# Kernel optimization log

Hardware: AMD Instinct MI355X
Metric: run time of the kernel (lower is better)

## Reference

```python
import jax, jax.numpy as jnp
import numpy as np

B, T, D, H = 2, 2048, 1024, 16
HS = D // H  # head_size = 64
DFF = 4 * D


def setup_inputs() -> dict:
    key = jax.random.key(0)
    ks = jax.random.split(key, 12)
    s = 0.02
    return {
        "x": jax.random.normal(ks[0], (B, T, D), dtype=jnp.float32),
        "Wq": jax.random.normal(ks[1], (D, D), dtype=jnp.float32) * s,
        "Wk": jax.random.normal(ks[2], (D, D), dtype=jnp.float32) * s,
        "Wv": jax.random.normal(ks[3], (D, D), dtype=jnp.float32) * s,
        "Wo": jax.random.normal(ks[4], (D, D), dtype=jnp.float32) * s,
        "bo": jnp.zeros((D,), dtype=jnp.float32),
        "W1": jax.random.normal(ks[5], (D, DFF), dtype=jnp.float32) * s,
        "b1": jnp.zeros((DFF,), dtype=jnp.float32),
        "W2": jax.random.normal(ks[6], (DFF, D), dtype=jnp.float32) * s,
        "b2": jnp.zeros((D,), dtype=jnp.float32),
        "g1": jnp.ones((D,), dtype=jnp.float32),
        "be1": jnp.zeros((D,), dtype=jnp.float32),
        "g2": jnp.ones((D,), dtype=jnp.float32),
        "be2": jnp.zeros((D,), dtype=jnp.float32),
    }


def layer_norm(x, g, b, eps=1e-5):
    mu = jnp.mean(x, axis=-1, keepdims=True)
    var = jnp.var(x, axis=-1, keepdims=True)
    return (x - mu) * jax.lax.rsqrt(var + eps) * g + b


def attention(x, Wq, Wk, Wv, Wo, bo):
    # x: [B,T,D] -> q,k,v: [B,H,T,HS]
    def split_heads(y):
        return y.reshape(B, T, H, HS).transpose(0, 2, 1, 3)
    q = split_heads(x @ Wq)
    k = split_heads(x @ Wk)
    v = split_heads(x @ Wv)
    scores = jnp.einsum("bhqd,bhkd->bhqk", q, k) / jnp.sqrt(jnp.float32(HS))
    causal = jnp.tril(jnp.ones((T, T), dtype=bool))
    scores = jnp.where(causal, scores, -jnp.inf)
    probs = jax.nn.softmax(scores, axis=-1)
    out = jnp.einsum("bhqk,bhkd->bhqd", probs, v)
    out = out.transpose(0, 2, 1, 3).reshape(B, T, D)
    return out @ Wo + bo


def reference(x, Wq, Wk, Wv, Wo, bo, W1, b1, W2, b2, g1, be1, g2, be2):
    x = x + attention(layer_norm(x, g1, be1), Wq, Wk, Wv, Wo, bo)
    h = layer_norm(x, g2, be2)
    x = x + (jax.nn.relu(h @ W1 + b1) @ W2 + b2)
    return x
```

## Files before the change

kernel.cpp:

```cpp
#include <hip/hip_runtime.h>
#include <stdint.h>

#define Bc   2
#define Tc   2048
#define Dc   1024
#define Hc   16
#define HSc  64
#define DFFc 4096
#define Mc   (Bc * Tc)

using f32x4 = __attribute__((ext_vector_type(4))) float;
using s16x8 = __attribute__((ext_vector_type(8))) short;

__device__ __forceinline__ ushort f2bf(float f) {
  union { float f; uint32_t u; } v; v.f = f;
  uint32_t r = (v.u + 0x7FFFu + ((v.u >> 16) & 1u)) >> 16;
  return (ushort)r;
}
__device__ __forceinline__ float bf2f(ushort u) {
  union { uint32_t u; float f; } v; v.u = ((uint32_t)u) << 16;
  return v.f;
}
__device__ __forceinline__ uint32_t cvtpk(float a, float b) {
  uint32_t r;
  asm volatile("v_cvt_pk_bf16_f32 %0, %1, %2" : "=v"(r) : "v"(a), "v"(b));
  return r;
}
__device__ __forceinline__ float wredsum(float v) {
#pragma unroll
  for (int o = 32; o > 0; o >>= 1) v += __shfl_down(v, o);
  return v;
}

__device__ __forceinline__ void gload16(const ushort* g, ushort* l) {
  __builtin_amdgcn_global_load_lds(
      (const __attribute__((address_space(1))) void*)g,
      (__attribute__((address_space(3))) void*)l, 16, 0, 0);
}

template <int N> __device__ __forceinline__ void vwait() {
  if constexpr (N == 0) asm volatile("s_waitcnt vmcnt(0)" ::: "memory");
  else if constexpr (N == 3) asm volatile("s_waitcnt vmcnt(3)" ::: "memory");
  else if constexpr (N == 4) asm volatile("s_waitcnt vmcnt(4)" ::: "memory");
  else if constexpr (N == 6) asm volatile("s_waitcnt vmcnt(6)" ::: "memory");
  else if constexpr (N == 8) asm volatile("s_waitcnt vmcnt(8)" ::: "memory");
}

__global__ __launch_bounds__(256) void tcast_all_kernel(
    const float* __restrict__ Wq, const float* __restrict__ Wk,
    const float* __restrict__ Wv, const float* __restrict__ Wo,
    const float* __restrict__ W1, const float* __restrict__ W2,
    ushort* __restrict__ wqkvt, ushort* __restrict__ wot,
    ushort* __restrict__ w1t, ushort* __restrict__ w2t) {
  __shared__ float t[32][33];
  const int id = blockIdx.x;
  const float* src; ushort* dst; int K, N, bx, by;
  if (id < 4096) {
    const int which = id >> 10, local = id & 1023;
    src = (which == 0) ? Wq : (which == 1) ? Wk : (which == 2) ? Wv : Wo;
    dst = (which == 3) ? wot : wqkvt + (size_t)which * 1024 * 1024;
    K = 1024; N = 1024; bx = local & 31; by = local >> 5;
  } else if (id < 8192) {
    const int local = id - 4096;
    src = W1; dst = w1t; K = 1024; N = 4096;
    bx = local & 127; by = local >> 7;
  } else {
    const int local = id - 8192;
    src = W2; dst = w2t; K = 4096; N = 1024;
    bx = local & 31; by = local >> 5;
  }
  const int tid = threadIdx.x;
  const int n0 = bx * 32, k0 = by * 32;
  const int r = tid >> 3, c4 = (tid & 7) * 4;
  const float4 v = *(const float4*)&src[(size_t)(k0 + r) * N + n0 + c4];
  t[r][c4] = v.x; t[r][c4 + 1] = v.y; t[r][c4 + 2] = v.z; t[r][c4 + 3] = v.w;
  __syncthreads();
  ushort4 o;
  o.x = f2bf(t[c4 + 0][r]); o.y = f2bf(t[c4 + 1][r]);
  o.z = f2bf(t[c4 + 2][r]); o.w = f2bf(t[c4 + 3][r]);
  *(ushort4*)&dst[(size_t)(n0 + r) * K + k0 + c4] = o;
}

__global__ __launch_bounds__(256) void ln_kernel(const float* __restrict__ x,
                                                 const float* __restrict__ g,
                                                 const float* __restrict__ b,
                                                 ushort* __restrict__ out) {
  const int row = blockIdx.x;
  const int tid = threadIdx.x;
  const int lane = tid & 63, wave = tid >> 6;
  const float4 v = ((const float4*)(x + (size_t)row * Dc))[tid];
  float s  = v.x + v.y + v.z + v.w;
  float s2 = v.x * v.x + v.y * v.y + v.z * v.z + v.w * v.w;
  __shared__ float rs[4], rs2[4];
  s = wredsum(s); s2 = wredsum(s2);
  if (lane == 0) { rs[wave] = s; rs2[wave] = s2; }
  __syncthreads();
  const float S  = rs[0] + rs[1] + rs[2] + rs[3];
  const float S2 = rs2[0] + rs2[1] + rs2[2] + rs2[3];
  const float mu = S * (1.f / (float)Dc);
  const float rstd = rsqrtf(S2 * (1.f / (float)Dc) - mu * mu + 1e-5f);
  const float4 gv = ((const float4*)g)[tid];
  const float4 bv = ((const float4*)b)[tid];
  ushort4 o;
  o.x = f2bf((v.x - mu) * rstd * gv.x + bv.x);
  o.y = f2bf((v.y - mu) * rstd * gv.y + bv.y);
  o.z = f2bf((v.z - mu) * rstd * gv.z + bv.z);
  o.w = f2bf((v.w - mu) * rstd * gv.w + bv.w);
  ((ushort4*)(out + (size_t)row * Dc))[tid] = o;
}

template <int BM, int NSPLIT, int OUT_BF16, int RELU, int BIAS, int RES, int QKVSPLIT>
__global__ __launch_bounds__(256) void gemm3_kernel(
    const ushort* __restrict__ A, const ushort* __restrict__ Bt,
    const float* __restrict__ bias, const float* __restrict__ res,
    void* __restrict__ C0, void* __restrict__ C1, void* __restrict__ C2,
    int M, int N, int K) {
  constexpr int MF = BM / 32;
  __shared__ __align__(16) ushort As[BM * 64];
  __shared__ __align__(16) ushort Bs[128 * 64];
  const int tid = threadIdx.x;
  const int lane = tid & 63, w = tid >> 6;
  const int wm = w >> 1, wn = w & 1;
  const int row0 = blockIdx.x * BM, col0 = blockIdx.y * 128;
  const int fr = lane & 15, fg = lane >> 4;
  const int kbeg = (NSPLIT > 1) ? blockIdx.z * (K / NSPLIT) : 0;
  const int kend = (NSPLIT > 1) ? kbeg + K / NSPLIT : K;

  f32x4 acc[MF][4] = {};

  for (int k0 = kbeg; k0 < kend; k0 += 64) {
#pragma unroll
    for (int i = 0; i < BM * 8 / 256; i++) {
      const int c = i * 256 + tid;
      const int r = c >> 3, j = c & 7;
      gload16(A + (size_t)(row0 + r) * K + k0 + ((j ^ (r & 7)) << 3),
              As + (i * 256 + w * 64) * 8);
    }
#pragma unroll
    for (int i = 0; i < 4; i++) {
      const int c = i * 256 + tid;
      const int r = c >> 3, j = c & 7;
      gload16(Bt + (size_t)(col0 + r) * K + k0 + ((j ^ (r & 7)) << 3),
              Bs + (i * 256 + w * 64) * 8);
    }
    __syncthreads();

#pragma unroll
    for (int kk = 0; kk < 2; kk++) {
      const int js = ((kk * 4 + fg) ^ (fr & 7)) << 3;
      s16x8 af[MF], bfr[4];
#pragma unroll
      for (int m = 0; m < MF; m++)
        af[m] = *(const s16x8*)&As[(wm * (BM / 2) + m * 16 + fr) * 64 + js];
#pragma unroll
      for (int n = 0; n < 4; n++)
        bfr[n] = *(const s16x8*)&Bs[(wn * 64 + n * 16 + fr) * 64 + js];
#pragma unroll
      for (int m = 0; m < MF; m++)
#pragma unroll
        for (int n = 0; n < 4; n++)
          acc[m][n] = __builtin_amdgcn_mfma_f32_16x16x32_bf16(af[m], bfr[n], acc[m][n], 0, 0, 0);
    }
    __syncthreads();
  }

  if (NSPLIT > 1) {
    float* P = (float*)C0 + (size_t)blockIdx.z * M * N;
#pragma unroll
    for (int m = 0; m < MF; m++)
#pragma unroll
      for (int n = 0; n < 4; n++)
#pragma unroll
        for (int i = 0; i < 4; i++) {
          const int r = row0 + wm * (BM / 2) + m * 16 + fg * 4 + i;
          const int c = col0 + n * 16 + wn * 64 + fr;
          P[(size_t)r * N + c] = acc[m][n][i];
        }
    return;
  }

  void* Cb = C0;
  int cbase = col0;
  if (QKVSPLIT) {
    const int which = col0 >> 10;
    Cb = (which == 0) ? C0 : (which == 1) ? C1 : C2;
    cbase = col0 & 1023;
  }
  const int NW = QKVSPLIT ? 1024 : N;
#pragma unroll
  for (int m = 0; m < MF; m++) {
#pragma unroll
    for (int n = 0; n < 4; n++) {
#pragma unroll
      for (int i = 0; i < 4; i++) {
        const int r = row0 + wm * (BM / 2) + m * 16 + fg * 4 + i;
        const int c = cbase + wn * 64 + n * 16 + fr;
        float v = acc[m][n][i];
        if (BIAS) v += bias[col0 - cbase + c];
        if (RELU) v = fmaxf(v, 0.f);
        if (RES)  v += res[(size_t)r * NW + c];
        if (OUT_BF16) ((ushort*)Cb)[(size_t)r * NW + c] = f2bf(v);
        else          ((float*)Cb)[(size_t)r * NW + c] = v;
      }
    }
  }
}

template <int BM, int NSPLIT, int OUT_BF16, int RELU, int BIAS, int RES, int QKVSPLIT>
__global__ __launch_bounds__(512, 2) void gemm8_kernel(
    const ushort* __restrict__ A, const ushort* __restrict__ Bt,
    const float* __restrict__ bias, const float* __restrict__ res,
    void* __restrict__ C0, void* __restrict__ C1, void* __restrict__ C2,
    int M, int N, int K) {
  constexpr int WR = BM / 2;
  constexpr int FI = WR / 16;
  constexpr int NPH = FI / 4;
  constexpr int APASS = BM / 128;
  constexpr int LPS = APASS + 2;
  constexpr int SLOT = (BM + 256) * 32;
  __shared__ __align__(16) ushort lds[4 * SLOT];

  const int tid = threadIdx.x;
  const int lane = tid & 63, w = tid >> 6;
  const int wm = w >> 2, wn = w & 3;
  const int fr = lane & 15, fg = lane >> 4;
  const int row0 = blockIdx.x * BM, col0 = blockIdx.y * 256;
  const int kbeg = (NSPLIT > 1) ? blockIdx.z * (K / NSPLIT) : 0;
  const int nt = (K / NSPLIT) / 32;

  const int scc = tid & 3;
  const int sr0 = tid >> 2;

  f32x4 acc[FI][4] = {};

  auto STAGE_A = [&](int t) {
    const int k0 = kbeg + t * 32;
    ushort* base = lds + (size_t)(t & 3) * SLOT;
#pragma unroll
    for (int i = 0; i < APASS; ++i) {
      const int r = i * 128 + sr0;
      const int j = scc ^ ((r >> 1) & 3);
      gload16(A + (size_t)(row0 + r) * K + k0 + j * 8,
              base + (i * 512 + w * 64) * 8);
    }
  };
  auto STAGE_B = [&](int t) {
    const int k0 = kbeg + t * 32;
    ushort* base = lds + (size_t)(t & 3) * SLOT + BM * 32;
#pragma unroll
    for (int i = 0; i < 2; ++i) {
      const int r = i * 128 + sr0;
      const int j = scc ^ ((r >> 1) & 3);
      gload16(Bt + (size_t)(col0 + r) * K + k0 + j * 8,
              base + (i * 512 + w * 64) * 8);
    }
  };

  STAGE_A(0); STAGE_B(0);
  STAGE_A(1); STAGE_B(1);
  STAGE_A(2); STAGE_B(2);
  vwait<2 * LPS>();
  __builtin_amdgcn_sched_barrier(0);
  __builtin_amdgcn_s_barrier();
  __builtin_amdgcn_sched_barrier(0);

  for (int s = 0; s < nt; ++s) {
    const ushort* sb = lds + (size_t)(s & 3) * SLOT;
    s16x8 bf[4];
#pragma unroll
    for (int ni = 0; ni < 4; ++ni) {
      const int rb = wn * 64 + ni * 16 + fr;
      const int ch = fg ^ ((rb >> 1) & 3);
      bf[ni] = *(const s16x8*)&sb[BM * 32 + rb * 32 + ch * 8];
    }
#pragma unroll
    for (int mh = 0; mh < NPH; ++mh) {
      s16x8 af[4];
#pragma unroll
      for (int mi = 0; mi < 4; ++mi) {
        const int ra = wm * WR + mh * 64 + mi * 16 + fr;
        const int ch = fg ^ ((ra >> 1) & 3);
        af[mi] = *(const s16x8*)&sb[ra * 32 + ch * 8];
      }
      if (s + 3 < nt) {
        if constexpr (NPH == 2) {
          if (mh == 0) STAGE_A(s + 3); else STAGE_B(s + 3);
        } else {
          STAGE_A(s + 3); STAGE_B(s + 3);
        }
      }
      __builtin_amdgcn_sched_barrier(0);
      __builtin_amdgcn_s_barrier();
      __builtin_amdgcn_sched_barrier(0);
      __builtin_amdgcn_s_setprio(1);
#pragma unroll
      for (int mi = 0; mi < 4; ++mi)
#pragma unroll
        for (int ni = 0; ni < 4; ++ni)
          acc[mh * 4 + mi][ni] = __builtin_amdgcn_mfma_f32_16x16x32_bf16(
              af[mi], bf[ni], acc[mh * 4 + mi][ni], 0, 0, 0);
      __builtin_amdgcn_s_setprio(0);
      __builtin_amdgcn_sched_barrier(0);
      if (mh == NPH - 1) {
        const int rem = nt - 2 - s;
        if (rem >= 2) vwait<2 * LPS>();
        else if (rem == 1) vwait<LPS>();
        else if (rem == 0) vwait<0>();
      }
      __builtin_amdgcn_s_barrier();
      __builtin_amdgcn_sched_barrier(0);
    }
  }

  if constexpr (NSPLIT > 1) {
    float* P = (float*)C0 + (size_t)blockIdx.z * M * N;
#pragma unroll
    for (int mi = 0; mi < FI; ++mi)
#pragma unroll
      for (int ni = 0; ni < 4; ++ni)
#pragma unroll
        for (int i = 0; i < 4; ++i) {
          const int r = row0 + wm * WR + mi * 16 + fg * 4 + i;
          const int c = col0 + wn * 64 + ni * 16 + fr;
          P[(size_t)r * N + c] = acc[mi][ni][i];
        }
  } else {
    void* Cb = C0;
    int cbase = col0;
    if (QKVSPLIT) {
      const int which = col0 >> 10;
      Cb = (which == 0) ? C0 : (which == 1) ? C1 : C2;
      cbase = col0 & 1023;
    }
    const int NW = QKVSPLIT ? 1024 : N;
#pragma unroll
    for (int mi = 0; mi < FI; ++mi) {
#pragma unroll
      for (int ni = 0; ni < 4; ++ni) {
#pragma unroll
        for (int i = 0; i < 4; ++i) {
          const int r = row0 + wm * WR + mi * 16 + fg * 4 + i;
          const int c = cbase + wn * 64 + ni * 16 + fr;
          float v = acc[mi][ni][i];
          if (BIAS) v += bias[col0 - cbase + c];
          if (RELU) v = fmaxf(v, 0.f);
          if (RES)  v += res[(size_t)r * NW + c];
          if (OUT_BF16) ((ushort*)Cb)[(size_t)r * NW + c] = f2bf(v);
          else          ((float*)Cb)[(size_t)r * NW + c] = v;
        }
      }
    }
  }
}

__global__ __launch_bounds__(256) void sum2_kernel(const float* __restrict__ p0,
                                                   const float* __restrict__ p1,
                                                   const float* __restrict__ bias,
                                                   const float* __restrict__ res,
                                                   float* __restrict__ out) {
  const size_t i = ((size_t)blockIdx.x * 256 + threadIdx.x) * 4;
  const float4 a = *(const float4*)(p0 + i);
  const float4 b = *(const float4*)(p1 + i);
  const float4 r = *(const float4*)(res + i);
  const float4 bs = *(const float4*)(bias + (i & 1023));
  float4 o;
  o.x = a.x + b.x + bs.x + r.x;
  o.y = a.y + b.y + bs.y + r.y;
  o.z = a.z + b.z + bs.z + r.z;
  o.w = a.w + b.w + bs.w + r.w;
  *(float4*)(out + i) = o;
}

__global__ __launch_bounds__(512) void fattn3_kernel(const ushort* __restrict__ Q,
                                                     const ushort* __restrict__ K,
                                                     const ushort* __restrict__ V,
                                                     float* __restrict__ pacc,
                                                     float* __restrict__ pl) {
  __shared__ __align__(16) ushort Kl[2][64][72];
  __shared__ __align__(16) ushort Vt[2][64][72];
  __shared__ __align__(16) uint32_t Pu[8][512];

  const int tid = threadIdx.x;
  const int lane = tid & 63, w = tid >> 6;
  const int fr = lane & 15, fg = lane >> 4;

  const int bh   = blockIdx.x & 31;
  const int rest = blockIdx.x >> 5;
  const int qb   = 15 - (rest >> 1);
  const int z    = rest & 1;
  const int h = bh & 15, b = bh >> 4;
  const int q0 = qb * 128;
  const size_t hbase = (size_t)b * Tc * Dc + (size_t)h * HSc;

  s16x8 qf0, qf1;
  {
    const ushort* qp = Q + hbase + (size_t)(q0 + w * 16 + fr) * Dc + fg * 8;
    qf0 = *(const s16x8*)(qp);
    qf1 = *(const s16x8*)(qp + 32);
  }

  const int kkey = tid >> 3, kd8 = (tid & 7) * 8;
  const int vkey = tid & 63, vd8 = (tid >> 6) * 8;

  const int t0 = z * (qb + 1), t1 = (z + 1) * (qb + 1);
  uint4 kreg = *(const uint4*)(K + hbase + (size_t)(t0 * 64 + kkey) * Dc + kd8);
  uint4 vreg = *(const uint4*)(V + hbase + (size_t)(t0 * 64 + vkey) * Dc + vd8);

  f32x4 acc[4] = {};
  float ps = 0.f;
  const float Cs = 0.18033688f;

  for (int kt = t0; kt < t1; kt++) {
    const int cur = (kt - t0) & 1;
    *(uint4*)&Kl[cur][kkey][kd8] = kreg;
    {
      union { uint4 v; ushort u[8]; } t; t.v = vreg;
#pragma unroll
      for (int j = 0; j < 8; j++) Vt[cur][vd8 + j][vkey] = t.u[j];
    }
    if (kt + 1 < t1) {
      kreg = *(const uint4*)(K + hbase + (size_t)((kt + 1) * 64 + kkey) * Dc + kd8);
      vreg = *(const uint4*)(V + hbase + (size_t)((kt + 1) * 64 + vkey) * Dc + vd8);
    }
    __syncthreads();

    const bool skip = (kt * 64 > q0 + w * 16 + 15);
    if (!skip) {
      f32x4 s[4] = {};
      __builtin_amdgcn_s_setprio(1);
#pragma unroll
      for (int kf = 0; kf < 4; kf++) {
        const s16x8 k0 = *(const s16x8*)&Kl[cur][kf * 16 + fr][fg * 8];
        const s16x8 k1 = *(const s16x8*)&Kl[cur][kf * 16 + fr][32 + fg * 8];
        s[kf] = __builtin_amdgcn_mfma_f32_16x16x32_bf16(k0, qf0, s[kf], 0, 0, 0);
        s[kf] = __builtin_amdgcn_mfma_f32_16x16x32_bf16(k1, qf1, s[kf], 0, 0, 0);
      }
      __builtin_amdgcn_s_setprio(0);

      const bool diag = (kt * 64 + 63 > q0 + w * 16);
      const int qg = q0 + w * 16 + fr;
#pragma unroll
      for (int kf = 0; kf < 4; kf++) {
        float p[4];
#pragma unroll
        for (int i = 0; i < 4; i++) {
          p[i] = exp2f(s[kf][i] * Cs);
          if (diag) {
            const int kg = kt * 64 + kf * 16 + fg * 4 + i;
            if (kg > qg) p[i] = 0.f;
          }
          ps += p[i];
        }
        uint2 pk;
        pk.x = cvtpk(p[0], p[1]);
        pk.y = cvtpk(p[2], p[3]);
        *(uint2*)&Pu[w][(2 * kf + (fg >> 1)) * 64 + fr * 4 + (fg & 1) * 2] = pk;
      }

      const s16x8 pa0 = *(const s16x8*)&Pu[w][fg * 64 + fr * 4];
      const s16x8 pa1 = *(const s16x8*)&Pu[w][(4 + fg) * 64 + fr * 4];
      __builtin_amdgcn_s_setprio(1);
#pragma unroll
      for (int df = 0; df < 4; df++) {
        const s16x8 v0 = *(const s16x8*)&Vt[cur][df * 16 + fr][fg * 8];
        const s16x8 v1 = *(const s16x8*)&Vt[cur][df * 16 + fr][32 + fg * 8];
        acc[df] = __builtin_amdgcn_mfma_f32_16x16x32_bf16(pa0, v0, acc[df], 0, 0, 0);
        acc[df] = __builtin_amdgcn_mfma_f32_16x16x32_bf16(pa1, v1, acc[df], 0, 0, 0);
      }
      __builtin_amdgcn_s_setprio(0);
    }
  }

  ps += __shfl_xor(ps, 16);
  ps += __shfl_xor(ps, 32);
  if (lane < 16)
    pl[(size_t)z * (32 * 2048) + (size_t)bh * 2048 + q0 + w * 16 + lane] = ps;

  float* pa = pacc + (size_t)z * (32ull * 2048 * 64) + (size_t)bh * 2048 * 64;
#pragma unroll
  for (int i = 0; i < 4; i++) {
    const int qr = q0 + w * 16 + fg * 4 + i;
#pragma unroll
    for (int df = 0; df < 4; df++)
      pa[(size_t)qr * 64 + df * 16 + fr] = acc[df][i];
  }
}

__global__ __launch_bounds__(256) void amerge_kernel(const float* __restrict__ pacc,
                                                     const float* __restrict__ pl,
                                                     ushort* __restrict__ O) {
  const int g = blockIdx.x * 256 + threadIdx.x;
  const int d4 = g & 15;
  const int t  = (g >> 4) & 2047;
  const int bh = g >> 15;
  const int h = bh & 15, b = bh >> 4;
  const size_t base = ((size_t)bh * 2048 + t) * 64 + d4 * 4;
  const float4 a = *(const float4*)(pacc + base);
  const float4 c = *(const float4*)(pacc + 32ull * 2048 * 64 + base);
  const float inv = 1.f / (pl[(size_t)bh * 2048 + t] + pl[32 * 2048 + (size_t)bh * 2048 + t]);
  ushort4 o;
  o.x = f2bf((a.x + c.x) * inv);
  o.y = f2bf((a.y + c.y) * inv);
  o.z = f2bf((a.z + c.z) * inv);
  o.w = f2bf((a.w + c.w) * inv);
  *(ushort4*)&O[((size_t)(b * 2048 + t)) * 1024 + h * 64 + d4 * 4] = o;
}

extern "C" void kernel_launch(void* const* d_in, const int* in_sizes, int n_in,
                              void* d_out, int out_size, void* d_ws, size_t ws_size,
                              hipStream_t stream) {
  const float* x   = (const float*)d_in[0];
  const float* Wq  = (const float*)d_in[1];
  const float* Wk  = (const float*)d_in[2];
  const float* Wv  = (const float*)d_in[3];
  const float* Wo  = (const float*)d_in[4];
  const float* bo  = (const float*)d_in[5];
  const float* W1  = (const float*)d_in[6];
  const float* b1  = (const float*)d_in[7];
  const float* W2  = (const float*)d_in[8];
  const float* b2  = (const float*)d_in[9];
  const float* g1  = (const float*)d_in[10];
  const float* be1 = (const float*)d_in[11];
  const float* g2  = (const float*)d_in[12];
  const float* be2 = (const float*)d_in[13];

  char* ws = (char*)d_ws;
  const size_t MB = 1ull << 20;
  ushort* ln1   = (ushort*)(ws + 0 * MB);
  ushort* qb    = (ushort*)(ws + 8 * MB);
  ushort* kb    = (ushort*)(ws + 16 * MB);
  ushort* vb    = (ushort*)(ws + 24 * MB);
  ushort* wqkvt = (ushort*)(ws + 32 * MB);
  ushort* wot   = (ushort*)(ws + 38 * MB);
  ushort* w1t   = (ushort*)(ws + 40 * MB);
  ushort* w2t   = (ushort*)(ws + 48 * MB);
  float*  x1    = (float*)(ws + 56 * MB);
  ushort* hb    = (ushort*)(ws + 72 * MB);
  float*  pacc  = (float*)(ws + 56 * MB);
  float*  plv   = (float*)(ws + 88 * MB);
  float*  fpart = (float*)(ws + 0 * MB);

  tcast_all_kernel<<<12288, 256, 0, stream>>>(Wq, Wk, Wv, Wo, W1, W2,
                                              wqkvt, wot, w1t, w2t);

  ln_kernel<<<Mc, 256, 0, stream>>>(x, g1, be1, ln1);

  gemm8_kernel<256, 1, 1, 0, 0, 0, 1><<<dim3(16, 12), 512, 0, stream>>>(
      ln1, wqkvt, nullptr, nullptr, qb, kb, vb, Mc, 3072, Dc);

  fattn3_kernel<<<1024, 512, 0, stream>>>(qb, kb, vb, pacc, plv);
  amerge_kernel<<<4096, 256, 0, stream>>>(pacc, plv, ln1);

  gemm3_kernel<64, 1, 0, 0, 1, 1, 0><<<dim3(64, 8), 256, 0, stream>>>(
      ln1, wot, bo, x, x1, nullptr, nullptr, Mc, Dc, Dc);

  ln_kernel<<<Mc, 256, 0, stream>>>(x1, g2, be2, qb);

  gemm8_kernel<256, 1, 1, 1, 1, 0, 0><<<dim3(16, 16), 512, 0, stream>>>(
      qb, w1t, b1, nullptr, hb, nullptr, nullptr, Mc, DFFc, Dc);

  gemm8_kernel<128, 2, 0, 0, 0, 0, 0><<<dim3(32, 4, 2), 512, 0, stream>>>(
      hb, w2t, nullptr, nullptr, fpart, nullptr, nullptr, Mc, Dc, DFFc);
  sum2_kernel<<<4096, 256, 0, stream>>>(fpart, fpart + (size_t)Mc * Dc, b2, x1,
                                        (float*)d_out);
}
```

Before: 214.4 us.

## Stage GEMM epilogue through LDS for vectorized bf16 stores, bf16 split-K partials

The gemm8 epilogue now packs accumulators to bf16 in a per-warp LDS staging tile and writes 16-byte vector rows to global memory, replacing scattered 2-byte stores. The split-K partials for the W2 GEMM are stored as bf16 instead of fp32, which halves the partial traffic, and the reduction kernel converts them back. The QKV GEMM tile size drops from 256 to 128 rows, doubling its grid. Rounding the partials to bf16 before summing costs accuracy in the FFN output. The old split-K path in gemm3 is removed.

```diff
diff --git a/kernel.cpp b/kernel.cpp
--- a/kernel.cpp
+++ b/kernel.cpp
@@ -43,7 +43,7 @@
   else if constexpr (N == 3) asm volatile("s_waitcnt vmcnt(3)" ::: "memory");
   else if constexpr (N == 4) asm volatile("s_waitcnt vmcnt(4)" ::: "memory");
   else if constexpr (N == 6) asm volatile("s_waitcnt vmcnt(6)" ::: "memory");
-  else if constexpr (N == 8) asm volatile("s_waitcnt vmcnt(8)" ::: "memory");
+  else asm volatile("s_waitcnt vmcnt(8)" ::: "memory");
 }
 
 __global__ __launch_bounds__(256) void tcast_all_kernel(
@@ -164,21 +164,6 @@
     __syncthreads();
   }
 
-  if (NSPLIT > 1) {
-    float* P = (float*)C0 + (size_t)blockIdx.z * M * N;
-#pragma unroll
-    for (int m = 0; m < MF; m++)
-#pragma unroll
-      for (int n = 0; n < 4; n++)
-#pragma unroll
-        for (int i = 0; i < 4; i++) {
-          const int r = row0 + wm * (BM / 2) + m * 16 + fg * 4 + i;
-          const int c = col0 + n * 16 + wn * 64 + fr;
-          P[(size_t)r * N + c] = acc[m][n][i];
-        }
-    return;
-  }
-
   void* Cb = C0;
   int cbase = col0;
   if (QKVSPLIT) {
@@ -312,8 +297,50 @@
     }
   }
 
-  if constexpr (NSPLIT > 1) {
-    float* P = (float*)C0 + (size_t)blockIdx.z * M * N;
+  __syncthreads();
+  if constexpr (NSPLIT > 1 || OUT_BF16) {
+    ushort* wst = lds + w * (WR * 64);
+#pragma unroll
+    for (int mi = 0; mi < FI; ++mi) {
+#pragma unroll
+      for (int ni = 0; ni < 4; ++ni) {
+#pragma unroll
+        for (int i = 0; i < 4; ++i) {
+          float v = acc[mi][ni][i];
+          if (NSPLIT == 1) {
+            if (BIAS) v += bias[col0 + wn * 64 + ni * 16 + fr];
+            if (RELU) v = fmaxf(v, 0.f);
+          }
+          wst[(mi * 16 + fg * 4 + i) * 64 + ni * 16 + fr] = f2bf(v);
+        }
+      }
+    }
+    const int rr = lane >> 3, cc = (lane & 7) * 8;
+    if constexpr (NSPLIT > 1) {
+      ushort* P = (ushort*)C0 + (size_t)blockIdx.z * M * N;
+#pragma unroll
+      for (int it = 0; it < WR / 8; ++it) {
+        const int r = it * 8 + rr;
+        *(uint4*)&P[(size_t)(row0 + wm * WR + r) * N + col0 + wn * 64 + cc] =
+            *(const uint4*)&wst[r * 64 + cc];
+      }
+    } else {
+      void* Cb = C0;
+      int cbase = col0;
+      if (QKVSPLIT) {
+        const int which = col0 >> 10;
+        Cb = (which == 0) ? C0 : (which == 1) ? C1 : C2;
+        cbase = col0 & 1023;
+      }
+      const int NW = QKVSPLIT ? 1024 : N;
+#pragma unroll
+      for (int it = 0; it < WR / 8; ++it) {
+        const int r = it * 8 + rr;
+        *(uint4*)&((ushort*)Cb)[(size_t)(row0 + wm * WR + r) * NW + cbase + wn * 64 + cc] =
+            *(const uint4*)&wst[r * 64 + cc];
+      }
+    }
+  } else {
 #pragma unroll
     for (int mi = 0; mi < FI; ++mi)
 #pragma unroll
@@ -322,52 +349,30 @@
         for (int i = 0; i < 4; ++i) {
           const int r = row0 + wm * WR + mi * 16 + fg * 4 + i;
           const int c = col0 + wn * 64 + ni * 16 + fr;
-          P[(size_t)r * N + c] = acc[mi][ni][i];
+          float v = acc[mi][ni][i];
+          if (BIAS) v += bias[c];
+          if (RELU) v = fmaxf(v, 0.f);
+          if (RES)  v += res[(size_t)r * N + c];
+          ((float*)C0)[(size_t)r * N + c] = v;
         }
-  } else {
-    void* Cb = C0;
-    int cbase = col0;
-    if (QKVSPLIT) {
-      const int which = col0 >> 10;
-      Cb = (which == 0) ? C0 : (which == 1) ? C1 : C2;
-      cbase = col0 & 1023;
-    }
-    const int NW = QKVSPLIT ? 1024 : N;
-#pragma unroll
-    for (int mi = 0; mi < FI; ++mi) {
-#pragma unroll
-      for (int ni = 0; ni < 4; ++ni) {
-#pragma unroll
-        for (int i = 0; i < 4; ++i) {
-          const int r = row0 + wm * WR + mi * 16 + fg * 4 + i;
-          const int c = cbase + wn * 64 + ni * 16 + fr;
-          float v = acc[mi][ni][i];
-          if (BIAS) v += bias[col0 - cbase + c];
-          if (RELU) v = fmaxf(v, 0.f);
-          if (RES)  v += res[(size_t)r * NW + c];
-          if (OUT_BF16) ((ushort*)Cb)[(size_t)r * NW + c] = f2bf(v);
-          else          ((float*)Cb)[(size_t)r * NW + c] = v;
-        }
-      }
-    }
-  }
-}
-
-__global__ __launch_bounds__(256) void sum2_kernel(const float* __restrict__ p0,
-                                                   const float* __restrict__ p1,
-                                                   const float* __restrict__ bias,
-                                                   const float* __restrict__ res,
-                                                   float* __restrict__ out) {
+  }
+}
+
+__global__ __launch_bounds__(256) void sum2b_kernel(const ushort* __restrict__ p,
+                                                    const float* __restrict__ bias,
+                                                    const float* __restrict__ res,
+                                                    float* __restrict__ out) {
   const size_t i = ((size_t)blockIdx.x * 256 + threadIdx.x) * 4;
-  const float4 a = *(const float4*)(p0 + i);
-  const float4 b = *(const float4*)(p1 + i);
+  const size_t MN = (size_t)Mc * Dc;
+  const ushort4 a = *(const ushort4*)(p + i);
+  const ushort4 b = *(const ushort4*)(p + MN + i);
   const float4 r = *(const float4*)(res + i);
   const float4 bs = *(const float4*)(bias + (i & 1023));
   float4 o;
-  o.x = a.x + b.x + bs.x + r.x;
-  o.y = a.y + b.y + bs.y + r.y;
-  o.z = a.z + b.z + bs.z + r.z;
-  o.w = a.w + b.w + bs.w + r.w;
+  o.x = bf2f(a.x) + bf2f(b.x) + bs.x + r.x;
+  o.y = bf2f(a.y) + bf2f(b.y) + bs.y + r.y;
+  o.z = bf2f(a.z) + bf2f(b.z) + bs.z + r.z;
+  o.w = bf2f(a.w) + bf2f(b.w) + bs.w + r.w;
   *(float4*)(out + i) = o;
 }
 
@@ -538,14 +543,14 @@
   ushort* hb    = (ushort*)(ws + 72 * MB);
   float*  pacc  = (float*)(ws + 56 * MB);
   float*  plv   = (float*)(ws + 88 * MB);
-  float*  fpart = (float*)(ws + 0 * MB);
+  ushort* fpart = (ushort*)(ws + 0 * MB);
 
   tcast_all_kernel<<<12288, 256, 0, stream>>>(Wq, Wk, Wv, Wo, W1, W2,
                                               wqkvt, wot, w1t, w2t);
 
   ln_kernel<<<Mc, 256, 0, stream>>>(x, g1, be1, ln1);
 
-  gemm8_kernel<256, 1, 1, 0, 0, 0, 1><<<dim3(16, 12), 512, 0, stream>>>(
+  gemm8_kernel<128, 1, 1, 0, 0, 0, 1><<<dim3(32, 12), 512, 0, stream>>>(
       ln1, wqkvt, nullptr, nullptr, qb, kb, vb, Mc, 3072, Dc);
 
   fattn3_kernel<<<1024, 512, 0, stream>>>(qb, kb, vb, pacc, plv);
@@ -561,6 +566,5 @@
 
   gemm8_kernel<128, 2, 0, 0, 0, 0, 0><<<dim3(32, 4, 2), 512, 0, stream>>>(
       hb, w2t, nullptr, nullptr, fpart, nullptr, nullptr, Mc, Dc, DFFc);
-  sum2_kernel<<<4096, 256, 0, stream>>>(fpart, fpart + (size_t)Mc * Dc, b2, x1,
-                                        (float*)d_out);
-}
+  sum2b_kernel<<<4096, 256, 0, stream>>>(fpart, b2, x1, (float*)d_out);
+}
```

New measurement: 215.4 us. Within noise of the previous version (+0.5%).
